# Performance work log

Hardware: AMD Instinct MI355X
Metric: run time of the kernel (lower is better)

The kernel has to match this reference:

```python
import jax, jax.numpy as jnp
import numpy as np

B, T = 64, 16            # batch, action horizon
ACTION_DIM = 32
HIDDEN = 1536            # config.input_embedding_dim
NUM_CAT = 4              # config.max_num_embodiments
NUM_BUCKETS = 1000       # config.num_timestep_buckets


def setup_inputs() -> dict:
    key = jax.random.key(0)
    ks = jax.random.split(key, 6)
    return {
        "actions": jax.random.normal(ks[0], (B, T, ACTION_DIM), jnp.float32),
        "timesteps": jax.random.randint(ks[1], (B,), 0, NUM_BUCKETS, dtype=jnp.int32),
        "cat_ids": jax.random.randint(ks[2], (B,), 0, NUM_CAT, dtype=jnp.int32),
        # CategorySpecificLinear params: W ~ 0.02*randn, b = zeros (as in torch init)
        "W1": 0.02 * jax.random.normal(ks[3], (NUM_CAT, ACTION_DIM, HIDDEN), jnp.float32),
        "b1": jnp.zeros((NUM_CAT, HIDDEN), jnp.float32),
        "W2": 0.02 * jax.random.normal(ks[4], (NUM_CAT, 2 * HIDDEN, HIDDEN), jnp.float32),
        "b2": jnp.zeros((NUM_CAT, HIDDEN), jnp.float32),
        "W3": 0.02 * jax.random.normal(ks[5], (NUM_CAT, HIDDEN, HIDDEN), jnp.float32),
        "b3": jnp.zeros((NUM_CAT, HIDDEN), jnp.float32),
    }


def cs_linear(x, W, b, onehot):
    """CategorySpecificLinear: equivalent to bmm(x, W[cat_ids]) + b[cat_ids].
    Grouped form avoids materializing the (B, Din, Dout) gathered weight tensor:
    compute per-category results (C=4 is tiny) and select via one-hot.
    x: (B,T,Din)  W: (C,Din,Dout)  b: (C,Dout)  onehot: (B,C)
    """
    y = jnp.einsum('btd,cdh->bcth', x, W)        # (B,C,T,Dout)
    y = jnp.einsum('bcth,bc->bth', y, onehot)    # select own category
    return y + (onehot @ b)[:, None, :]


def sinusoidal_pe(t, dim):
    """Standard sinusoidal positional encoding of scalar positions t (B,T) -> (B,T,dim)."""
    half = dim // 2
    freqs = jnp.exp(-np.log(10000.0) * jnp.arange(half, dtype=jnp.float32) / half)
    ang = t.astype(jnp.float32)[..., None] * freqs  # (B,T,half)
    return jnp.concatenate([jnp.sin(ang), jnp.cos(ang)], axis=-1)


def reference(actions, timesteps, cat_ids, W1, b1, W2, b2, W3, b3):
    onehot = jax.nn.one_hot(cat_ids, W1.shape[0], dtype=actions.dtype)  # (B,C)
    t = jnp.broadcast_to(timesteps[:, None], actions.shape[:2])          # (B,T)
    a_emb = cs_linear(actions, W1, b1, onehot)                            # (B,T,H)
    tau_emb = sinusoidal_pe(t, a_emb.shape[-1]).astype(a_emb.dtype)       # (B,T,H)
    x = jnp.concatenate([a_emb, tau_emb], axis=-1)                        # (B,T,2H)
    h = cs_linear(x, W2, b2, onehot)
    h = h * jax.nn.sigmoid(h)                                             # swish
    return cs_linear(h, W3, b3, onehot)                                   # (B,T,H)
```

## Files before the change

### kernel.cpp

```cpp
#include <hip/hip_runtime.h>
#include <hip/hip_bf16.h>

#define BB 64
#define TT 16
#define ROWS 1024
#define ADIM 32
#define HID 1536
#define NCAT 4
#define MT_MAX 20

typedef __attribute__((ext_vector_type(8))) short bf16x8;
typedef __attribute__((ext_vector_type(4))) float f32x4;

static __device__ __forceinline__ unsigned short f2bf(float f) {
    union { float f; unsigned int u; } v; v.f = f;
    unsigned int u = v.u + 0x7fff + ((v.u >> 16) & 1);
    return (unsigned short)(u >> 16);
}

__global__ void prep_kernel(const int* __restrict__ cat_ids,
                            int* __restrict__ msample, int* __restrict__ mcat) {
    __shared__ int counts[NCAT];
    const int t = threadIdx.x;
    if (t < NCAT) {
        int c = 0;
        for (int s = 0; s < BB; ++s) c += (cat_ids[s] == t);
        counts[t] = c;
    }
    __syncthreads();
    if (t < NCAT) {
        int off = 0;
        for (int c = 0; c < t; ++c) off += (counts[c] + 3) >> 2;
        const int mt = (counts[t] + 3) >> 2;
        int idx = 0;
        for (int s = 0; s < BB; ++s)
            if (cat_ids[s] == t) msample[off * 4 + (idx++)] = s;
        for (; idx < mt * 4; ++idx) msample[off * 4 + idx] = -1;
        for (int mm = 0; mm < mt; ++mm) mcat[off + mm] = t;
    }
    __syncthreads();
    if (t == 0) {
        int tot = 0;
        for (int c = 0; c < NCAT; ++c) tot += (counts[c] + 3) >> 2;
        for (int mm = tot; mm < MT_MAX; ++mm) mcat[mm] = -1;
    }
}

__global__ void build_x_kernel(const float* __restrict__ actions,
                               const int* __restrict__ timesteps,
                               const int* __restrict__ cat_ids,
                               const float* __restrict__ W1,
                               const float* __restrict__ b1,
                               unsigned short* __restrict__ X) {
    const int s = blockIdx.x;
    const int part = blockIdx.y;
    const int t = threadIdx.x;
    if (part < 6) {
        const int cat = cat_ids[s];
        const int h = part * 256 + t;
        __shared__ float act[TT][ADIM];
        const float* ab = actions + (size_t)s * TT * ADIM;
        ((float*)act)[t]       = ab[t];
        ((float*)act)[t + 256] = ab[t + 256];
        __syncthreads();
        const float* W1c = W1 + (size_t)cat * ADIM * HID + h;
        float acc[TT];
        #pragma unroll
        for (int r = 0; r < TT; ++r) acc[r] = 0.f;
        #pragma unroll 8
        for (int d = 0; d < ADIM; ++d) {
            const float wv = W1c[(size_t)d * HID];
            #pragma unroll
            for (int r = 0; r < TT; ++r) acc[r] += act[r][d] * wv;
        }
        const float bias = b1[cat * HID + h];
        #pragma unroll
        for (int r = 0; r < TT; ++r)
            X[(size_t)(s * TT + r) * (2 * HID) + h] = f2bf(acc[r] + bias);
    } else {
        const float ts = (float)timesteps[s];
        #pragma unroll
        for (int j = 0; j < 6; ++j) {
            const int i = j * 256 + t;
            const int ii = (i < 768) ? i : i - 768;
            const float freq = expf(-9.210340371976184f * (float)ii * (1.0f / 768.0f));
            const float ang = ts * freq;
            const float v = (i < 768) ? sinf(ang) : cosf(ang);
            const unsigned short bv = f2bf(v);
            for (int r = 0; r < TT; ++r)
                X[(size_t)(s * TT + r) * (2 * HID) + HID + i] = bv;
        }
    }
}

template<int K, int KSPLIT>
__global__ __launch_bounds__(64, 2) void gemm_sw(
        const unsigned short* __restrict__ Xin,
        const float* __restrict__ W,
        const int* __restrict__ msample,
        const int* __restrict__ mcat,
        float* __restrict__ P) {
    constexpr int KP = K / KSPLIT;
    constexpr int NT = KP / 32;
    static_assert(NT % 3 == 0, "NT must be divisible by 3");

    const int m   = blockIdx.y;
    const int cat = mcat[m];
    if (cat < 0) return;
    const int n0 = blockIdx.x * 64;
    const int ks = blockIdx.z;
    const int k0 = ks * KP;

    const int l   = threadIdx.x;
    const int col = l & 15;
    const int g   = l >> 4;

    int sidx[4];
    #pragma unroll
    for (int f = 0; f < 4; ++f) sidx[f] = msample[m * 4 + f];

    const unsigned short* aptr[4];
    #pragma unroll
    for (int f = 0; f < 4; ++f) {
        const int s = sidx[f] < 0 ? 0 : sidx[f];
        aptr[f] = Xin + ((size_t)s * TT + col) * K + k0 + g * 8;
    }
    const float* wptr = W + ((size_t)cat * K + k0 + g * 8) * HID + n0 + col;

    f32x4 acc[4][4];
    #pragma unroll
    for (int i = 0; i < 4; ++i)
        #pragma unroll
        for (int j = 0; j < 4; ++j) acc[i][j] = f32x4{0.f, 0.f, 0.f, 0.f};

    float  bs[3][32];
    bf16x8 as[3][4];

    auto issueB = [&](int t, int s) {
        const int tc = (t < NT) ? t : NT - 1;
        #pragma unroll
        for (int nf = 0; nf < 4; ++nf)
            #pragma unroll
            for (int j = 0; j < 8; ++j)
                bs[s][nf * 8 + j] = wptr[(size_t)(tc * 32 + j) * HID + nf * 16];
    };
    auto issueA = [&](int t, int s) {
        const int tc = (t < NT) ? t : NT - 1;
        #pragma unroll
        for (int f = 0; f < 4; ++f)
            as[s][f] = *(const bf16x8*)(aptr[f] + tc * 32);
    };
    auto step = [&](int s) {
        bf16x8 bfr[4];
        #pragma unroll
        for (int nf = 0; nf < 4; ++nf)
            #pragma unroll
            for (int j = 0; j < 8; ++j)
                bfr[nf][j] = (short)f2bf(bs[s][nf * 8 + j]);
        #pragma unroll
        for (int mf = 0; mf < 4; ++mf)
            #pragma unroll
            for (int nf = 0; nf < 4; ++nf)
                acc[mf][nf] = __builtin_amdgcn_mfma_f32_16x16x32_bf16(
                    as[s][mf], bfr[nf], acc[mf][nf], 0, 0, 0);
    };

    issueB(0, 0); issueA(0, 0);
    issueB(1, 1); issueA(1, 1);

    for (int tt = 0; tt < NT; tt += 3) {
        issueB(tt + 2, 2); issueA(tt + 2, 2);
        step(0);
        issueB(tt + 3, 0); issueA(tt + 3, 0);
        step(1);
        issueB(tt + 4, 1); issueA(tt + 4, 1);
        step(2);
    }

    #pragma unroll
    for (int mf = 0; mf < 4; ++mf) {
        if (sidx[mf] < 0) continue;
        float* prow = P + ((size_t)ks * ROWS + (size_t)sidx[mf] * TT + g * 4) * HID
                        + n0 + col;
        #pragma unroll
        for (int nf = 0; nf < 4; ++nf)
            #pragma unroll
            for (int r = 0; r < 4; ++r)
                prow[(size_t)r * HID + nf * 16] = acc[mf][nf][r];
    }
}

template<int S, bool DOSWISH, bool BF16OUT>
__global__ void finish_kernel(const float* __restrict__ P,
                              const float* __restrict__ bias,
                              const int* __restrict__ cat_ids,
                              void* __restrict__ out) {
    const int idx = blockIdx.x * 256 + threadIdx.x;
    const int i4 = idx * 4;
    const int row = i4 / HID;
    const int colb = i4 - row * HID;
    const int cat = cat_ids[row >> 4];
    float4 v = *(const float4*)(P + i4);
    #pragma unroll
    for (int s2 = 1; s2 < S; ++s2) {
        const float4 p = *(const float4*)(P + (size_t)s2 * ROWS * HID + i4);
        v.x += p.x; v.y += p.y; v.z += p.z; v.w += p.w;
    }
    const float4 bv = *(const float4*)(bias + (size_t)cat * HID + colb);
    v.x += bv.x; v.y += bv.y; v.z += bv.z; v.w += bv.w;
    if (DOSWISH) {
        v.x = v.x / (1.f + __expf(-v.x));
        v.y = v.y / (1.f + __expf(-v.y));
        v.z = v.z / (1.f + __expf(-v.z));
        v.w = v.w / (1.f + __expf(-v.w));
    }
    if (BF16OUT) {
        uint2 u;
        u.x = (unsigned)f2bf(v.x) | ((unsigned)f2bf(v.y) << 16);
        u.y = (unsigned)f2bf(v.z) | ((unsigned)f2bf(v.w) << 16);
        *(uint2*)((unsigned short*)out + i4) = u;
    } else {
        *(float4*)((float*)out + i4) = v;
    }
}

extern "C" void kernel_launch(void* const* d_in, const int* in_sizes, int n_in,
                              void* d_out, int out_size, void* d_ws, size_t ws_size,
                              hipStream_t stream) {
    const float* actions   = (const float*)d_in[0];
    const int*   timesteps = (const int*)d_in[1];
    const int*   cat_ids   = (const int*)d_in[2];
    const float* W1        = (const float*)d_in[3];
    const float* b1        = (const float*)d_in[4];
    const float* W2        = (const float*)d_in[5];
    const float* b2        = (const float*)d_in[6];
    const float* W3        = (const float*)d_in[7];
    const float* b3        = (const float*)d_in[8];

    char* ws = (char*)d_ws;
    unsigned short* X = (unsigned short*)ws;
    unsigned short* H = (unsigned short*)(ws + 6291456);
    float* P          = (float*)(ws + 9437184);
    int* msample      = (int*)(ws + 34603008);
    int* mcat         = msample + MT_MAX * 4;

    prep_kernel<<<1, 64, 0, stream>>>(cat_ids, msample, mcat);
    build_x_kernel<<<dim3(BB, 7), 256, 0, stream>>>(actions, timesteps, cat_ids, W1, b1, X);

    gemm_sw<2 * HID, 4><<<dim3(HID / 64, MT_MAX, 4), 64, 0, stream>>>(
        X, W2, msample, mcat, P);
    finish_kernel<4, true, true><<<ROWS * HID / 4 / 256, 256, 0, stream>>>(
        P, b2, cat_ids, H);

    gemm_sw<HID, 2><<<dim3(HID / 64, MT_MAX, 2), 64, 0, stream>>>(
        H, W3, msample, mcat, P);
    finish_kernel<2, false, false><<<ROWS * HID / 4 / 256, 256, 0, stream>>>(
        P, b3, cat_ids, d_out);
}
```

Before: 119.6 us.

## Drop split-K and fuse bias/swish epilogue into grouped GEMM kernels

Removes the K-split partial-sum buffer and the separate finish kernels. Each GEMM block now computes the full K reduction and applies bias, swish and the bf16 conversion in its epilogue, with a 1D grid remapped so neighbouring blocks are spread across XCDs. This saves the partial-sum writes and reads and two kernel launches. In exchange there are 4x and 2x fewer blocks, each with a longer serial K loop, so parallelism and latency hiding drop. Launch bounds also change to 1 and weight conversion switches to the library RNE cast.

```diff
diff --git a/kernel.cpp b/kernel.cpp
--- a/kernel.cpp
+++ b/kernel.cpp
@@ -8,6 +8,8 @@
 #define HID 1536
 #define NCAT 4
 #define MT_MAX 20
+#define NTILE 24
+#define GRID_G (MT_MAX * NTILE)
 
 typedef __attribute__((ext_vector_type(8))) short bf16x8;
 typedef __attribute__((ext_vector_type(4))) float f32x4;
@@ -16,6 +18,10 @@
     union { float f; unsigned int u; } v; v.f = f;
     unsigned int u = v.u + 0x7fff + ((v.u >> 16) & 1);
     return (unsigned short)(u >> 16);
+}
+static __device__ __forceinline__ short f2bf_rne(float f) {
+    __hip_bfloat16 h = __float2bfloat16(f);
+    return __builtin_bit_cast(short, h);
 }
 
 __global__ void prep_kernel(const int* __restrict__ cat_ids,
@@ -93,23 +99,24 @@
     }
 }
 
-template<int K, int KSPLIT>
-__global__ __launch_bounds__(64, 2) void gemm_sw(
+template<int K, bool SWISH, bool BF16OUT>
+__global__ __launch_bounds__(64, 1) void gemm_fused(
         const unsigned short* __restrict__ Xin,
         const float* __restrict__ W,
+        const float* __restrict__ bias,
         const int* __restrict__ msample,
         const int* __restrict__ mcat,
-        float* __restrict__ P) {
-    constexpr int KP = K / KSPLIT;
-    constexpr int NT = KP / 32;
+        void* __restrict__ Out) {
+    constexpr int NT = K / 32;
     static_assert(NT % 3 == 0, "NT must be divisible by 3");
 
-    const int m   = blockIdx.y;
+    const int id  = blockIdx.x;
+    const int g60 = (id & 7) * (GRID_G / 8) + (id >> 3);
+    const int m   = g60 / NTILE;
+    const int nt  = g60 - m * NTILE;
     const int cat = mcat[m];
     if (cat < 0) return;
-    const int n0 = blockIdx.x * 64;
-    const int ks = blockIdx.z;
-    const int k0 = ks * KP;
+    const int n0 = nt * 64;
 
     const int l   = threadIdx.x;
     const int col = l & 15;
@@ -123,9 +130,9 @@
     #pragma unroll
     for (int f = 0; f < 4; ++f) {
         const int s = sidx[f] < 0 ? 0 : sidx[f];
-        aptr[f] = Xin + ((size_t)s * TT + col) * K + k0 + g * 8;
-    }
-    const float* wptr = W + ((size_t)cat * K + k0 + g * 8) * HID + n0 + col;
+        aptr[f] = Xin + ((size_t)s * TT + col) * K + g * 8;
+    }
+    const float* wptr = W + ((size_t)cat * K + g * 8) * HID + n0 + col;
 
     f32x4 acc[4][4];
     #pragma unroll
@@ -137,18 +144,19 @@
     bf16x8 as[3][4];
 
     auto issueB = [&](int t, int s) {
-        const int tc = (t < NT) ? t : NT - 1;
+        if (t >= NT) return;
+        const float* wp = wptr + (size_t)t * 32 * HID;
         #pragma unroll
         for (int nf = 0; nf < 4; ++nf)
             #pragma unroll
             for (int j = 0; j < 8; ++j)
-                bs[s][nf * 8 + j] = wptr[(size_t)(tc * 32 + j) * HID + nf * 16];
+                bs[s][nf * 8 + j] = wp[(size_t)j * HID + nf * 16];
     };
     auto issueA = [&](int t, int s) {
-        const int tc = (t < NT) ? t : NT - 1;
+        if (t >= NT) return;
         #pragma unroll
         for (int f = 0; f < 4; ++f)
-            as[s][f] = *(const bf16x8*)(aptr[f] + tc * 32);
+            as[s][f] = *(const bf16x8*)(aptr[f] + t * 32);
     };
     auto step = [&](int s) {
         bf16x8 bfr[4];
@@ -156,7 +164,7 @@
         for (int nf = 0; nf < 4; ++nf)
             #pragma unroll
             for (int j = 0; j < 8; ++j)
-                bfr[nf][j] = (short)f2bf(bs[s][nf * 8 + j]);
+                bfr[nf][j] = f2bf_rne(bs[s][nf * 8 + j]);
         #pragma unroll
         for (int mf = 0; mf < 4; ++mf)
             #pragma unroll
@@ -167,7 +175,6 @@
 
     issueB(0, 0); issueA(0, 0);
     issueB(1, 1); issueA(1, 1);
-
     for (int tt = 0; tt < NT; tt += 3) {
         issueB(tt + 2, 2); issueA(tt + 2, 2);
         step(0);
@@ -177,50 +184,23 @@
         step(2);
     }
 
+    const float* bc = bias + (size_t)cat * HID + n0 + col;
     #pragma unroll
     for (int mf = 0; mf < 4; ++mf) {
         if (sidx[mf] < 0) continue;
-        float* prow = P + ((size_t)ks * ROWS + (size_t)sidx[mf] * TT + g * 4) * HID
-                        + n0 + col;
-        #pragma unroll
-        for (int nf = 0; nf < 4; ++nf)
-            #pragma unroll
-            for (int r = 0; r < 4; ++r)
-                prow[(size_t)r * HID + nf * 16] = acc[mf][nf][r];
-    }
-}
-
-template<int S, bool DOSWISH, bool BF16OUT>
-__global__ void finish_kernel(const float* __restrict__ P,
-                              const float* __restrict__ bias,
-                              const int* __restrict__ cat_ids,
-                              void* __restrict__ out) {
-    const int idx = blockIdx.x * 256 + threadIdx.x;
-    const int i4 = idx * 4;
-    const int row = i4 / HID;
-    const int colb = i4 - row * HID;
-    const int cat = cat_ids[row >> 4];
-    float4 v = *(const float4*)(P + i4);
-    #pragma unroll
-    for (int s2 = 1; s2 < S; ++s2) {
-        const float4 p = *(const float4*)(P + (size_t)s2 * ROWS * HID + i4);
-        v.x += p.x; v.y += p.y; v.z += p.z; v.w += p.w;
-    }
-    const float4 bv = *(const float4*)(bias + (size_t)cat * HID + colb);
-    v.x += bv.x; v.y += bv.y; v.z += bv.z; v.w += bv.w;
-    if (DOSWISH) {
-        v.x = v.x / (1.f + __expf(-v.x));
-        v.y = v.y / (1.f + __expf(-v.y));
-        v.z = v.z / (1.f + __expf(-v.z));
-        v.w = v.w / (1.f + __expf(-v.w));
-    }
-    if (BF16OUT) {
-        uint2 u;
-        u.x = (unsigned)f2bf(v.x) | ((unsigned)f2bf(v.y) << 16);
-        u.y = (unsigned)f2bf(v.z) | ((unsigned)f2bf(v.w) << 16);
-        *(uint2*)((unsigned short*)out + i4) = u;
-    } else {
-        *(float4*)((float*)out + i4) = v;
+        const size_t rowbase = (size_t)sidx[mf] * TT + g * 4;
+        #pragma unroll
+        for (int nf = 0; nf < 4; ++nf) {
+            const float bv = bc[nf * 16];
+            #pragma unroll
+            for (int r = 0; r < 4; ++r) {
+                float v = acc[mf][nf][r] + bv;
+                if (SWISH) v = v / (1.f + __expf(-v));
+                const size_t off = (rowbase + r) * HID + n0 + nf * 16 + col;
+                if (BF16OUT) ((unsigned short*)Out)[off] = f2bf(v);
+                else         ((float*)Out)[off] = v;
+            }
+        }
     }
 }
 
@@ -240,20 +220,14 @@
     char* ws = (char*)d_ws;
     unsigned short* X = (unsigned short*)ws;
     unsigned short* H = (unsigned short*)(ws + 6291456);
-    float* P          = (float*)(ws + 9437184);
-    int* msample      = (int*)(ws + 34603008);
+    int* msample      = (int*)(ws + 9437184);
     int* mcat         = msample + MT_MAX * 4;
 
     prep_kernel<<<1, 64, 0, stream>>>(cat_ids, msample, mcat);
     build_x_kernel<<<dim3(BB, 7), 256, 0, stream>>>(actions, timesteps, cat_ids, W1, b1, X);
 
-    gemm_sw<2 * HID, 4><<<dim3(HID / 64, MT_MAX, 4), 64, 0, stream>>>(
-        X, W2, msample, mcat, P);
-    finish_kernel<4, true, true><<<ROWS * HID / 4 / 256, 256, 0, stream>>>(
-        P, b2, cat_ids, H);
-
-    gemm_sw<HID, 2><<<dim3(HID / 64, MT_MAX, 2), 64, 0, stream>>>(
-        H, W3, msample, mcat, P);
-    finish_kernel<2, false, false><<<ROWS * HID / 4 / 256, 256, 0, stream>>>(
-        P, b3, cat_ids, d_out);
-}
+    gemm_fused<2 * HID, true, true><<<GRID_G, 64, 0, stream>>>(
+        X, W2, b2, msample, mcat, H);
+    gemm_fused<HID, false, false><<<GRID_G, 64, 0, stream>>>(
+        H, W3, b3, msample, mcat, d_out);
+}
```

New measurement: 137.5 us. 15.0% more time.
